# Performance work log

Hardware: AMD Instinct MI355X
Metric: run time of the kernel (lower is better)

The kernel has to match this reference:

```python
import jax, jax.numpy as jnp
import numpy as np
from jax import lax

T = 64
TAU = 2.0
ALPHA = 4.0  # spikingjelly surrogate.Sigmoid default
V_TH = 1.0

@jax.custom_vjp
def spike(v):
    # Heaviside(v) with sigmoid surrogate gradient
    return (v >= 0.0).astype(v.dtype)

def _spike_fwd(v):
    return spike(v), v

def _spike_bwd(v, g):
    s = jax.nn.sigmoid(ALPHA * v)
    return (g * ALPHA * s * (1.0 - s),)

spike.defvjp(_spike_fwd, _spike_bwd)

def setup_inputs() -> dict:
    key = jax.random.key(0)
    k1, k2, k3 = jax.random.split(key, 3)
    x = jax.random.normal(k1, (2048, 28, 28), dtype=jnp.float32)
    W1 = jax.random.normal(k2, (1024, 784), dtype=jnp.float32) * (1.0 / np.sqrt(784))
    W2 = jax.random.normal(k3, (10, 1024), dtype=jnp.float32) * (1.0 / np.sqrt(1024))
    return {"x": x, "W1": W1, "W2": W2}

def _lif_step(v, c):
    # decay_input=True: v += (x - (v - v_reset)) / tau, v_reset = 0
    v = v + (c - v) / TAU
    s = spike(v - V_TH)
    v = v * (1.0 - s)  # hard reset to 0
    return v, s

def reference(x, W1, W2):
    B = x.shape[0]
    xf = x.reshape(B, -1)                      # [B, 784]
    c1 = xf @ W1.T                              # [B, 1024], identical every timestep
    v1_0 = jnp.zeros((B, W1.shape[0]), x.dtype)
    v2_0 = jnp.zeros((B, W2.shape[0]), x.dtype)

    def step(carry, _):
        v1, v2 = carry
        v1, s1 = _lif_step(v1, c1)              # [B, 1024]
        c2 = s1 @ W2.T                          # [B, 10]
        v2, s2 = _lif_step(v2, c2)              # [B, 10]
        return (v1, v2), s2

    _, out = lax.scan(step, (v1_0, v2_0), None, length=T)
    return out  # [T, B, 10]
```

## Files before the change

kernel.cpp:

```cpp
#include <hip/hip_runtime.h>
#include <stdint.h>

typedef unsigned long long u64;
typedef unsigned int u32;

#define T_STEPS 64
#define KDIM 784
#define N1 1024
#define NB 2048
#define N2 10

__global__ __launch_bounds__(256) void k_prep(
    const float* __restrict__ X, float* __restrict__ Xt,
    const float* __restrict__ W1, float* __restrict__ W1t,
    const float* __restrict__ W2, float* __restrict__ W2T)
{
    int b = blockIdx.x;
    if (b == 2400) {
        for (int it = 0; it < 4; ++it) {
            int j = it * 256 + threadIdx.x;
            float r[12];
#pragma unroll
            for (int i = 0; i < 10; ++i) r[i] = W2[i * N1 + j];
            r[10] = 0.f; r[11] = 0.f;
#pragma unroll
            for (int i = 0; i < 12; ++i) W2T[j * 12 + i] = r[i];
        }
        return;
    }
    __shared__ float t[32][33];
    const float* src; float* dst; int R;
    int tile_r, tile_c;
    if (b < 1600) { src = X;  dst = Xt;  R = NB; tile_r = b / 25; tile_c = b % 25; }
    else { b -= 1600; src = W1; dst = W1t; R = N1; tile_r = b / 25; tile_c = b % 25; }

    const int tx = threadIdx.x & 31, ty = threadIdx.x >> 5;
    const int r0 = tile_r << 5, c0 = tile_c << 5;

#pragma unroll
    for (int i = 0; i < 32; i += 8) {
        int c = c0 + tx;
        t[ty + i][tx] = (c < KDIM) ? src[(size_t)(r0 + ty + i) * KDIM + c] : 0.f;
    }
    __syncthreads();
#pragma unroll
    for (int i = 0; i < 32; i += 8) {
        int c = c0 + ty + i;
        if (c < KDIM) dst[(size_t)c * R + r0 + tx] = t[tx][ty + i];
    }
}

__global__ __launch_bounds__(256, 2) void k_gemm_lif1(
    const float* __restrict__ Xt,
    const float* __restrict__ W1t,
    u64* __restrict__ bits)
{
    const int tid = threadIdx.x;
    const int tx  = tid & 15;
    const int ty  = tid >> 4;
    const int bm  = blockIdx.y << 6;
    const int bn  = blockIdx.x << 6;

#define LOAD_A(k) (*(const float4*)(Xt  + (size_t)(k) * NB + bm + (ty << 2)))
#define LOAD_B(k) (*(const float4*)(W1t + (size_t)(k) * N1 + bn + (tx << 2)))
#define FMAS(av, bv)                                                                      \
    acc[0][0] = fmaf(av.x, bv.x, acc[0][0]); acc[0][1] = fmaf(av.x, bv.y, acc[0][1]);     \
    acc[0][2] = fmaf(av.x, bv.z, acc[0][2]); acc[0][3] = fmaf(av.x, bv.w, acc[0][3]);     \
    acc[1][0] = fmaf(av.y, bv.x, acc[1][0]); acc[1][1] = fmaf(av.y, bv.y, acc[1][1]);     \
    acc[1][2] = fmaf(av.y, bv.z, acc[1][2]); acc[1][3] = fmaf(av.y, bv.w, acc[1][3]);     \
    acc[2][0] = fmaf(av.z, bv.x, acc[2][0]); acc[2][1] = fmaf(av.z, bv.y, acc[2][1]);     \
    acc[2][2] = fmaf(av.z, bv.z, acc[2][2]); acc[2][3] = fmaf(av.z, bv.w, acc[2][3]);     \
    acc[3][0] = fmaf(av.w, bv.x, acc[3][0]); acc[3][1] = fmaf(av.w, bv.y, acc[3][1]);     \
    acc[3][2] = fmaf(av.w, bv.z, acc[3][2]); acc[3][3] = fmaf(av.w, bv.w, acc[3][3]);

    float acc[4][4];
#pragma unroll
    for (int r = 0; r < 4; ++r)
#pragma unroll
        for (int c = 0; c < 4; ++c) acc[r][c] = 0.f;

    float4 pa[16], pb[16];
#pragma unroll
    for (int q = 0; q < 16; ++q) { pa[q] = LOAD_A(q); pb[q] = LOAD_B(q); }

    for (int t = 0; t < 48; ++t) {
#pragma unroll
        for (int q = 0; q < 16; ++q) {
            float4 av = pa[q], bv = pb[q];
            pa[q] = LOAD_A(t * 16 + 16 + q);
            pb[q] = LOAD_B(t * 16 + 16 + q);
            FMAS(av, bv);
        }
    }
#pragma unroll
    for (int q = 0; q < 16; ++q) {
        float4 av = pa[q], bv = pb[q];
        FMAS(av, bv);
    }
#undef LOAD_A
#undef LOAD_B
#undef FMAS

    float c[16], v[16];
    u32 blo[16], bhi[16];
#pragma unroll
    for (int u = 0; u < 16; ++u) {
        c[u] = acc[u >> 2][u & 3];
        v[u] = 0.f; blo[u] = 0u; bhi[u] = 0u;
    }
    for (int t = 0; t < 32; ++t) {
#pragma unroll
        for (int u = 0; u < 16; ++u) {
            v[u] += (c[u] - v[u]) * 0.5f;
            bool s = v[u] >= 1.0f;
            blo[u] |= (s ? 1u : 0u) << t;
            v[u] = s ? 0.f : v[u];
        }
    }
    for (int t = 0; t < 32; ++t) {
#pragma unroll
        for (int u = 0; u < 16; ++u) {
            v[u] += (c[u] - v[u]) * 0.5f;
            bool s = v[u] >= 1.0f;
            bhi[u] |= (s ? 1u : 0u) << t;
            v[u] = s ? 0.f : v[u];
        }
    }
#pragma unroll
    for (int u = 0; u < 16; ++u) {
        int r = u >> 2, cc = u & 3;
        bits[(size_t)(bm + (ty << 2) + r) * N1 + (bn + (tx << 2) + cc)] =
            ((u64)bhi[u] << 32) | (u64)blo[u];
    }
}

__global__ __launch_bounds__(256) void k_c2lif(
    const u64* __restrict__ bits, const float* __restrict__ W2T,
    float* __restrict__ out)
{
    __shared__ u64   masksS[N1];
    __shared__ u32   idxS[N1];
    __shared__ float wS[4][64][12];
    __shared__ float c2S[4][64][12];
    __shared__ float c2r[64][12];
    __shared__ float s2S[64][10];

    const int tid  = threadIdx.x;
    const int w    = tid >> 6;
    const int lane = tid & 63;
    const int b    = blockIdx.x;

    const u64* row = bits + (size_t)b * N1;
    const int base_j = w << 8;

    u64 mm[4];
#pragma unroll
    for (int q = 0; q < 4; ++q) mm[q] = row[base_j + (q << 6) + lane];

    int nact = 0;
#pragma unroll
    for (int q = 0; q < 4; ++q) {
        u64 ball = __ballot(mm[q] != 0ULL);
        int pos = nact + __popcll(ball & ((1ULL << lane) - 1ULL));
        if (mm[q] != 0ULL) { masksS[base_j + pos] = mm[q]; idxS[base_j + pos] = base_j + (q << 6) + lane; }
        nact += __popcll(ball);
    }
    const int npad = (nact + 3) & ~3;
    if (lane < npad - nact) { masksS[base_j + nact + lane] = 0ULL; idxS[base_j + nact + lane] = 0u; }
    asm volatile("s_waitcnt lgkmcnt(0)" ::: "memory");

    float acc[10];
#pragma unroll
    for (int i = 0; i < 10; ++i) acc[i] = 0.f;

    for (int base = 0; base < npad; base += 64) {
        const int cnt = min(64, npad - base);
        if (lane < cnt) {
            int j = (int)idxS[base_j + base + lane];
            const float4* src = (const float4*)(W2T + j * 12);
            float4 a = src[0], bq = src[1], cq = src[2];
            *(float4*)&wS[w][lane][0] = a;
            *(float4*)&wS[w][lane][4] = bq;
            *(float4*)&wS[w][lane][8] = cq;
        }
        asm volatile("s_waitcnt lgkmcnt(0) vmcnt(0)" ::: "memory");
        __builtin_amdgcn_sched_barrier(0);

        for (int a = 0; a < cnt; a += 4) {
            u64 m[4];
#pragma unroll
            for (int q = 0; q < 4; ++q) m[q] = masksS[base_j + base + a + q];
#pragma unroll
            for (int q = 0; q < 4; ++q) {
                float sf = (float)((m[q] >> lane) & 1ULL);
                const float* wr = &wS[w][a + q][0];
                float4 w0 = *(const float4*)(wr);
                float4 w1 = *(const float4*)(wr + 4);
                float2 w2 = *(const float2*)(wr + 8);
                acc[0] = fmaf(sf, w0.x, acc[0]); acc[1] = fmaf(sf, w0.y, acc[1]);
                acc[2] = fmaf(sf, w0.z, acc[2]); acc[3] = fmaf(sf, w0.w, acc[3]);
                acc[4] = fmaf(sf, w1.x, acc[4]); acc[5] = fmaf(sf, w1.y, acc[5]);
                acc[6] = fmaf(sf, w1.z, acc[6]); acc[7] = fmaf(sf, w1.w, acc[7]);
                acc[8] = fmaf(sf, w2.x, acc[8]); acc[9] = fmaf(sf, w2.y, acc[9]);
            }
        }
    }

#pragma unroll
    for (int i = 0; i < 10; ++i) c2S[w][lane][i] = acc[i];
    __syncthreads();

    for (int idx = tid; idx < 64 * 10; idx += 256) {
        int t = idx / 10, i = idx % 10;
        c2r[t][i] = ((c2S[0][t][i] + c2S[1][t][i]) + c2S[2][t][i]) + c2S[3][t][i];
    }
    __syncthreads();

    if (tid < 10) {
        const int i = tid;
        float v2 = 0.f;
        for (int tb = 0; tb < 64; tb += 8) {
            float cc[8];
#pragma unroll
            for (int q = 0; q < 8; ++q) cc[q] = c2r[tb + q][i];
#pragma unroll
            for (int q = 0; q < 8; ++q) {
                v2 += (cc[q] - v2) * 0.5f;
                bool s = v2 >= 1.0f;
                s2S[tb + q][i] = s ? 1.f : 0.f;
                v2 = s ? 0.f : v2;
            }
        }
    }
    __syncthreads();

    for (int idx = tid; idx < 64 * 10; idx += 256) {
        int t = idx / 10, i = idx % 10;
        out[(size_t)t * (NB * N2) + (size_t)b * N2 + i] = s2S[t][i];
    }
}

extern "C" void kernel_launch(void* const* d_in, const int* in_sizes, int n_in,
                              void* d_out, int out_size, void* d_ws, size_t ws_size,
                              hipStream_t stream) {
    const float* X  = (const float*)d_in[0];
    const float* W1 = (const float*)d_in[1];
    const float* W2 = (const float*)d_in[2];
    float* out = (float*)d_out;

    char* ws = (char*)d_ws;
    u64*   bits = (u64*)ws;
    float* W2T  = (float*)(ws + (size_t)NB * N1 * 8);
    float* Xt   = (float*)(ws + (size_t)NB * N1 * 8 + 65536);
    float* W1t  = Xt + (size_t)KDIM * NB;

    k_prep<<<dim3(2401), dim3(256), 0, stream>>>(X, Xt, W1, W1t, W2, W2T);

    dim3 g1(N1 / 64, NB / 64);
    k_gemm_lif1<<<g1, dim3(256), 0, stream>>>(Xt, W1t, bits);

    k_c2lif<<<dim3(NB), dim3(256), 0, stream>>>(bits, W2T, out);
}
```

Baseline: 201.8 us.

## Stage GEMM tiles into LDS via async global_load_lds with 4-buffer pipeline

Replaces the register-prefetched direct global loads in the first GEMM with shared-memory tiles filled by global_load_lds (direct-to-LDS) into a 4-deep ring, staying two k-steps ahead, with a barrier each step. Operands are shared across the block instead of each thread loading its own float4s from global, so redundant global traffic and register pressure drop, and launch bounds are relaxed. It adds per-step barriers and depends on vmcnt counting and the LDS layout being correct.

```diff
diff --git a/kernel.cpp b/kernel.cpp
--- a/kernel.cpp
+++ b/kernel.cpp
@@ -50,28 +50,67 @@
     }
 }
 
-__global__ __launch_bounds__(256, 2) void k_gemm_lif1(
+#define NSTEP (KDIM / 16)
+
+typedef const __attribute__((address_space(1))) void gas_void;
+typedef __attribute__((address_space(3))) void las_void;
+
+__global__ __launch_bounds__(256) void k_gemm_lif1(
     const float* __restrict__ Xt,
     const float* __restrict__ W1t,
     u64* __restrict__ bits)
 {
-    const int tid = threadIdx.x;
-    const int tx  = tid & 15;
-    const int ty  = tid >> 4;
-    const int bm  = blockIdx.y << 6;
-    const int bn  = blockIdx.x << 6;
-
-#define LOAD_A(k) (*(const float4*)(Xt  + (size_t)(k) * NB + bm + (ty << 2)))
-#define LOAD_B(k) (*(const float4*)(W1t + (size_t)(k) * N1 + bn + (tx << 2)))
-#define FMAS(av, bv)                                                                      \
-    acc[0][0] = fmaf(av.x, bv.x, acc[0][0]); acc[0][1] = fmaf(av.x, bv.y, acc[0][1]);     \
-    acc[0][2] = fmaf(av.x, bv.z, acc[0][2]); acc[0][3] = fmaf(av.x, bv.w, acc[0][3]);     \
-    acc[1][0] = fmaf(av.y, bv.x, acc[1][0]); acc[1][1] = fmaf(av.y, bv.y, acc[1][1]);     \
-    acc[1][2] = fmaf(av.y, bv.z, acc[1][2]); acc[1][3] = fmaf(av.y, bv.w, acc[1][3]);     \
-    acc[2][0] = fmaf(av.z, bv.x, acc[2][0]); acc[2][1] = fmaf(av.z, bv.y, acc[2][1]);     \
-    acc[2][2] = fmaf(av.z, bv.z, acc[2][2]); acc[2][3] = fmaf(av.z, bv.w, acc[2][3]);     \
-    acc[3][0] = fmaf(av.w, bv.x, acc[3][0]); acc[3][1] = fmaf(av.w, bv.y, acc[3][1]);     \
-    acc[3][2] = fmaf(av.w, bv.z, acc[3][2]); acc[3][3] = fmaf(av.w, bv.w, acc[3][3]);
+    __shared__ __align__(16) float A2[4][16][64];
+    __shared__ __align__(16) float B2[4][16][64];
+
+    const int tid  = threadIdx.x;
+    const int lane = tid & 63;
+    const int tx   = tid & 15;
+    const int ty   = tid >> 4;
+    const int bm   = blockIdx.y << 6;
+    const int bn   = blockIdx.x << 6;
+
+    const int w4   = __builtin_amdgcn_readfirstlane((tid >> 6) << 2);
+    const int srow = w4 + (lane >> 4);
+    const int scol = (lane & 15) << 2;
+
+    const float* gA = Xt  + (size_t)srow * NB + bm + scol;
+    const float* gB = W1t + (size_t)srow * N1 + bn + scol;
+
+#define STAGE(pp, t)                                                          \
+    {                                                                         \
+        __builtin_amdgcn_global_load_lds((gas_void*)(gA + (size_t)(t) * (16 * NB)), \
+                                         (las_void*)&A2[pp][w4][0], 16, 0, 0); \
+        __builtin_amdgcn_global_load_lds((gas_void*)(gB + (size_t)(t) * (16 * N1)), \
+                                         (las_void*)&B2[pp][w4][0], 16, 0, 0); \
+    }
+
+#define COMPUTE(CUR)                                                          \
+    _Pragma("unroll")                                                         \
+    for (int kk = 0; kk < 16; ++kk) {                                         \
+        float4 av = *(const float4*)(&A2[CUR][kk][ty << 2]);                  \
+        float4 bv = *(const float4*)(&B2[CUR][kk][tx << 2]);                  \
+        acc[0][0] = fmaf(av.x, bv.x, acc[0][0]); acc[0][1] = fmaf(av.x, bv.y, acc[0][1]); \
+        acc[0][2] = fmaf(av.x, bv.z, acc[0][2]); acc[0][3] = fmaf(av.x, bv.w, acc[0][3]); \
+        acc[1][0] = fmaf(av.y, bv.x, acc[1][0]); acc[1][1] = fmaf(av.y, bv.y, acc[1][1]); \
+        acc[1][2] = fmaf(av.y, bv.z, acc[1][2]); acc[1][3] = fmaf(av.y, bv.w, acc[1][3]); \
+        acc[2][0] = fmaf(av.z, bv.x, acc[2][0]); acc[2][1] = fmaf(av.z, bv.y, acc[2][1]); \
+        acc[2][2] = fmaf(av.z, bv.z, acc[2][2]); acc[2][3] = fmaf(av.z, bv.w, acc[2][3]); \
+        acc[3][0] = fmaf(av.w, bv.x, acc[3][0]); acc[3][1] = fmaf(av.w, bv.y, acc[3][1]); \
+        acc[3][2] = fmaf(av.w, bv.z, acc[3][2]); acc[3][3] = fmaf(av.w, bv.w, acc[3][3]); \
+    }
+
+#define BODY(T, U)                                                            \
+    {                                                                         \
+        asm volatile("s_waitcnt vmcnt(2)" ::: "memory");                      \
+        __builtin_amdgcn_sched_barrier(0);                                    \
+        __builtin_amdgcn_s_barrier();                                         \
+        __builtin_amdgcn_sched_barrier(0);                                    \
+        if ((T) + 2 < NSTEP) STAGE(((U) + 2) & 3, (T) + 2);                   \
+        __builtin_amdgcn_sched_barrier(0);                                    \
+        COMPUTE((U));                                                         \
+        __builtin_amdgcn_sched_barrier(0);                                    \
+    }
 
     float acc[4][4];
 #pragma unroll
@@ -79,27 +118,24 @@
 #pragma unroll
         for (int c = 0; c < 4; ++c) acc[r][c] = 0.f;
 
-    float4 pa[16], pb[16];
-#pragma unroll
-    for (int q = 0; q < 16; ++q) { pa[q] = LOAD_A(q); pb[q] = LOAD_B(q); }
-
-    for (int t = 0; t < 48; ++t) {
-#pragma unroll
-        for (int q = 0; q < 16; ++q) {
-            float4 av = pa[q], bv = pb[q];
-            pa[q] = LOAD_A(t * 16 + 16 + q);
-            pb[q] = LOAD_B(t * 16 + 16 + q);
-            FMAS(av, bv);
-        }
-    }
-#pragma unroll
-    for (int q = 0; q < 16; ++q) {
-        float4 av = pa[q], bv = pb[q];
-        FMAS(av, bv);
-    }
-#undef LOAD_A
-#undef LOAD_B
-#undef FMAS
+    STAGE(0, 0);
+    STAGE(1, 1);
+
+    for (int tt = 0; tt < 12; ++tt) {
+        const int t0 = tt << 2;
+        BODY(t0 + 0, 0);
+        BODY(t0 + 1, 1);
+        BODY(t0 + 2, 2);
+        BODY(t0 + 3, 3);
+    }
+    asm volatile("s_waitcnt vmcnt(0)" ::: "memory");
+    __builtin_amdgcn_sched_barrier(0);
+    __builtin_amdgcn_s_barrier();
+    __builtin_amdgcn_sched_barrier(0);
+    COMPUTE(0);
+#undef BODY
+#undef STAGE
+#undef COMPUTE
 
     float c[16], v[16];
     u32 blo[16], bhi[16];
```

Result: no change. 201.5 us (-0.1%).
